# Performance work log

Hardware: AMD Instinct MI355X
Metric: run time of the kernel (lower is better)

## Reference

```python
import jax, jax.numpy as jnp
import numpy as np

NEG_SLOPE = 0.2
EPS = 1e-16


def _gat_layer(x, src, dst, W, a_src, a_dst, b, n_nodes):
    # x: [N, Fin], W: [Fout, Fin]; src/dst: [E'] (self-loops already appended)
    h = x @ W.T                              # [N, Fout]
    alpha_s = h @ a_src                      # [N] per-source score
    alpha_d = h @ a_dst                      # [N] per-dest score
    e = jax.nn.leaky_relu(alpha_s[src] + alpha_d[dst], NEG_SLOPE)  # [E']
    # segment softmax over destination nodes (PyG softmax semantics)
    m = jax.ops.segment_max(e, dst, num_segments=n_nodes)          # [N]
    ex = jnp.exp(e - m[dst])                                       # [E']
    s = jax.ops.segment_sum(ex, dst, num_segments=n_nodes)         # [N]
    alpha = ex / (s[dst] + EPS)                                    # [E']
    out = jax.ops.segment_sum(alpha[:, None] * h[src], dst, num_segments=n_nodes)
    return out + b, alpha


def setup_inputs() -> dict:
    key = jax.random.key(0)
    ks = jax.random.split(key, 14)
    N, E, F_IN, H1, H2, F_OUT = 50000, 800000, 128, 64, 64, 32
    sc = 0.1
    return {
        "x": jax.random.normal(ks[0], (N, F_IN), dtype=jnp.float32),
        "edge_index": jax.random.randint(ks[1], (2, E), 0, N, dtype=jnp.int64),
        "W1": jax.random.normal(ks[2], (H1, F_IN), dtype=jnp.float32) * sc,
        "a_src1": jax.random.normal(ks[3], (H1,), dtype=jnp.float32) * sc,
        "a_dst1": jax.random.normal(ks[4], (H1,), dtype=jnp.float32) * sc,
        "b1": jnp.zeros((H1,), dtype=jnp.float32),
        "W2": jax.random.normal(ks[5], (H2, H1), dtype=jnp.float32) * sc,
        "a_src2": jax.random.normal(ks[6], (H2,), dtype=jnp.float32) * sc,
        "a_dst2": jax.random.normal(ks[7], (H2,), dtype=jnp.float32) * sc,
        "b2": jnp.zeros((H2,), dtype=jnp.float32),
        "W3": jax.random.normal(ks[8], (F_OUT, H2), dtype=jnp.float32) * sc,
        "a_src3": jax.random.normal(ks[9], (F_OUT,), dtype=jnp.float32) * sc,
        "a_dst3": jax.random.normal(ks[10], (F_OUT,), dtype=jnp.float32) * sc,
        "b3": jnp.zeros((F_OUT,), dtype=jnp.float32),
    }


def reference(x, edge_index, W1, a_src1, a_dst1, b1, W2, a_src2, a_dst2, b2, W3, a_src3, a_dst3, b3):
    N = x.shape[0]
    loops = jnp.arange(N, dtype=edge_index.dtype)
    src = jnp.concatenate([edge_index[0], loops])  # add_self_loops=True
    dst = jnp.concatenate([edge_index[1], loops])

    h, alpha1 = _gat_layer(x, src, dst, W1, a_src1, a_dst1, b1, N)
    h = jax.nn.relu(h)
    h, _ = _gat_layer(h, src, dst, W2, a_src2, a_dst2, b2, N)
    h = jax.nn.relu(h)
    out, _ = _gat_layer(h, src, dst, W3, a_src3, a_dst3, b3, N)
    # att_tuple = (edge_index with self loops, attention coefficients of layer 1)
    return (jnp.stack([src, dst]), alpha1, out)
```

## Files before the change

kernel.cpp:

```cpp
#include <hip/hip_runtime.h>
#include <hip/hip_bf16.h>
#include <math.h>

#define NEG_SLOPE 0.2f
#define GAT_EPS 1e-16f

constexpr int NN = 50000;
constexpr int NE = 800000;
constexpr int EP = NE + NN;
constexpr int NB = (NN + 255) / 256;

__device__ inline void edge_sd(const int* __restrict__ ei, int i, int& s, int& d) {
    if (i < NE) { s = ei[i]; d = ei[NE + i]; }
    else        { s = d = i - NE; }
}

__device__ inline float bflo(unsigned int h) { return __uint_as_float(h << 16); }
__device__ inline float bfhi(unsigned int h) { return __uint_as_float(h & 0xffff0000u); }

__global__ void k_edges_hist(const int* __restrict__ ei, float* __restrict__ out0,
                             int* __restrict__ cnt, int* __restrict__ rank) {
    int i = blockIdx.x * blockDim.x + threadIdx.x;
    if (i >= EP) return;
    int s, d; edge_sd(ei, i, s, d);
    __builtin_nontemporal_store((float)s, &out0[i]);
    __builtin_nontemporal_store((float)d, &out0[EP + i]);
    int r = atomicAdd(&cnt[d], 1);
    __builtin_nontemporal_store(r, &rank[i]);
}

__global__ void k_scan1(const int* __restrict__ cnt, int* __restrict__ rowptr,
                        int* __restrict__ bsum) {
    __shared__ int sh[256];
    int t = threadIdx.x, i = blockIdx.x * 256 + t;
    int v = (i < NN) ? cnt[i] : 0;
    sh[t] = v; __syncthreads();
    for (int off = 1; off < 256; off <<= 1) {
        int x = (t >= off) ? sh[t - off] : 0;
        __syncthreads();
        sh[t] += x;
        __syncthreads();
    }
    if (i < NN) rowptr[i] = sh[t] - v;
    if (t == 255) bsum[blockIdx.x] = sh[255];
}

__global__ void k_scan2(int* __restrict__ bsum, int* __restrict__ boff) {
    __shared__ int sh[256];
    int t = threadIdx.x;
    int v = (t < NB) ? bsum[t] : 0;
    sh[t] = v; __syncthreads();
    for (int off = 1; off < 256; off <<= 1) {
        int x = (t >= off) ? sh[t - off] : 0;
        __syncthreads();
        sh[t] += x;
        __syncthreads();
    }
    if (t < NB) boff[t] = sh[t] - v;
}

__global__ void k_scan3(int* __restrict__ rowptr, const int* __restrict__ boff) {
    int i = blockIdx.x * blockDim.x + threadIdx.x;
    if (i < NN) rowptr[i] += boff[i >> 8];
    if (i == 0) rowptr[NN] = EP;
}

__global__ void k_fill(const int* __restrict__ ei, const int* __restrict__ rank,
                       const int* __restrict__ rowptr, int* __restrict__ col) {
    int i = blockIdx.x * blockDim.x + threadIdx.x;
    if (i >= EP) return;
    int s, d; edge_sd(ei, i, s, d);
    int pos = rowptr[d] + rank[i];
    __builtin_nontemporal_store(s, &col[pos]);
}

__global__ void k_alpha_out(const int* __restrict__ ei, const float* __restrict__ as_,
                            const float* __restrict__ ad_, const float* __restrict__ inv,
                            float* __restrict__ out_alpha) {
    int i = blockIdx.x * blockDim.x + threadIdx.x;
    if (i >= EP) return;
    int s, d; edge_sd(ei, i, s, d);
    float v = as_[s] + ad_[d];
    v = v > 0.f ? v : NEG_SLOPE * v;
    __builtin_nontemporal_store(__expf(v) * inv[d], &out_alpha[i]);
}

struct alignas(8) bh4 { __hip_bfloat16 a, b, c, d; };

__device__ inline void fma4(float4& acc, float x, const float4& w) {
    acc.x = fmaf(x, w.x, acc.x);
    acc.y = fmaf(x, w.y, acc.y);
    acc.z = fmaf(x, w.z, acc.z);
    acc.w = fmaf(x, w.w, acc.w);
}

template <int FIN, int FOUT, int NPB>
__global__ __launch_bounds__(256) void k_gemm_t(const float* __restrict__ in,
                                                const float* __restrict__ W,
                                                const float* __restrict__ avs,
                                                const float* __restrict__ avd,
                                                __hip_bfloat16* __restrict__ H,
                                                float* __restrict__ as_,
                                                float* __restrict__ ad_, int n) {
    constexpr int TF = FOUT / 4;
    constexpr int XS = FIN + 4;
    constexpr int WS = FOUT + 4;
    __shared__ float sX[NPB * XS];
    __shared__ float sWt[FIN * WS];
    int tid = threadIdx.x;
    for (int idx = tid; idx < FIN * FOUT; idx += 256) {
        int f = idx % FOUT, k = idx / FOUT;
        sWt[k * WS + f] = W[f * FIN + k];
    }
    int nb = blockIdx.x * NPB;
    for (int idx = tid; idx < NPB * (FIN / 4); idx += 256) {
        int node = idx / (FIN / 4), kq = idx % (FIN / 4);
        int g = nb + node;
        float4 v = make_float4(0.f, 0.f, 0.f, 0.f);
        if (g < n) v = *(const float4*)&in[(size_t)g * FIN + kq * 4];
        *(float4*)&sX[node * XS + kq * 4] = v;
    }
    __syncthreads();

    int fq = tid % TF, ng = tid / TF;
    int n0 = ng * 4;
    float4 acc0 = make_float4(0.f, 0.f, 0.f, 0.f);
    float4 acc1 = acc0, acc2 = acc0, acc3 = acc0;
    for (int k = 0; k < FIN; k += 4) {
        float4 w0 = *(const float4*)&sWt[(k + 0) * WS + fq * 4];
        float4 w1 = *(const float4*)&sWt[(k + 1) * WS + fq * 4];
        float4 w2 = *(const float4*)&sWt[(k + 2) * WS + fq * 4];
        float4 w3 = *(const float4*)&sWt[(k + 3) * WS + fq * 4];
        float4 x0 = *(const float4*)&sX[(n0 + 0) * XS + k];
        float4 x1 = *(const float4*)&sX[(n0 + 1) * XS + k];
        float4 x2 = *(const float4*)&sX[(n0 + 2) * XS + k];
        float4 x3 = *(const float4*)&sX[(n0 + 3) * XS + k];
        fma4(acc0, x0.x, w0); fma4(acc0, x0.y, w1); fma4(acc0, x0.z, w2); fma4(acc0, x0.w, w3);
        fma4(acc1, x1.x, w0); fma4(acc1, x1.y, w1); fma4(acc1, x1.z, w2); fma4(acc1, x1.w, w3);
        fma4(acc2, x2.x, w0); fma4(acc2, x2.y, w1); fma4(acc2, x2.z, w2); fma4(acc2, x2.w, w3);
        fma4(acc3, x3.x, w0); fma4(acc3, x3.y, w1); fma4(acc3, x3.z, w2); fma4(acc3, x3.w, w3);
    }
    float4 accs[4] = {acc0, acc1, acc2, acc3};
    float4 vs4 = *(const float4*)&avs[fq * 4];
    float4 vd4 = *(const float4*)&avd[fq * 4];
#pragma unroll
    for (int j = 0; j < 4; ++j) {
        int g = nb + n0 + j;
        float ps = accs[j].x * vs4.x + accs[j].y * vs4.y + accs[j].z * vs4.z + accs[j].w * vs4.w;
        float pd = accs[j].x * vd4.x + accs[j].y * vd4.y + accs[j].z * vd4.z + accs[j].w * vd4.w;
#pragma unroll
        for (int off = TF / 2; off; off >>= 1) {
            ps += __shfl_down(ps, off, TF);
            pd += __shfl_down(pd, off, TF);
        }
        if (g < n) {
            if (fq == 0) { as_[g] = ps; ad_[g] = pd; }
            bh4 o;
            o.a = __float2bfloat16(accs[j].x);
            o.b = __float2bfloat16(accs[j].y);
            o.c = __float2bfloat16(accs[j].z);
            o.d = __float2bfloat16(accs[j].w);
            *(bh4*)&H[(size_t)g * FOUT + fq * 4] = o;
        }
    }
}

template <int FOUT, bool RELU, bool WRITE_INV>
__global__ __launch_bounds__(256) void k_node_attn(
    const int* __restrict__ rowptr, const int* __restrict__ col,
    const float* __restrict__ as_, const float* __restrict__ ad_,
    const __hip_bfloat16* __restrict__ H, const float* __restrict__ bias,
    float* __restrict__ outp, float* __restrict__ inv_out) {
    int wid = (blockIdx.x * blockDim.x + threadIdx.x) >> 6;
    int lane = threadIdx.x & 63;
    if (wid >= NN) return;
    int start = rowptr[wid], end = rowptr[wid + 1];
    float adv = ad_[wid];
    const unsigned int* __restrict__ H2 = (const unsigned int*)H;

    float sloc = 0.f;
    float ax = 0.f, ay = 0.f;
    for (int c = start; c < end; c += 64) {
        int e = c + lane;
        float p = 0.f;
        int sc = 0;
        if (e < end) {
            sc = col[e];
            float v = as_[sc] + adv;
            v = v > 0.f ? v : NEG_SLOPE * v;
            p = __expf(v);
        }
        sloc += p;
        int cnt = end - c; if (cnt > 64) cnt = 64;
        if (FOUT == 64) {
            int half = lane >> 5, fl = lane & 31;
            int j = 0;
            for (; j + 8 <= cnt; j += 8) {
                int e0 = j + half, e1 = j + 2 + half, e2 = j + 4 + half, e3 = j + 6 + half;
                float p0 = __shfl(p, e0), p1 = __shfl(p, e1);
                float p2 = __shfl(p, e2), p3 = __shfl(p, e3);
                int s0 = __shfl(sc, e0), s1 = __shfl(sc, e1);
                int s2 = __shfl(sc, e2), s3 = __shfl(sc, e3);
                unsigned int h0 = H2[((size_t)s0 << 5) + fl];
                unsigned int h1 = H2[((size_t)s1 << 5) + fl];
                unsigned int h2 = H2[((size_t)s2 << 5) + fl];
                unsigned int h3 = H2[((size_t)s3 << 5) + fl];
                ax = fmaf(p0, bflo(h0), ax); ay = fmaf(p0, bfhi(h0), ay);
                ax = fmaf(p1, bflo(h1), ax); ay = fmaf(p1, bfhi(h1), ay);
                ax = fmaf(p2, bflo(h2), ax); ay = fmaf(p2, bfhi(h2), ay);
                ax = fmaf(p3, bflo(h3), ax); ay = fmaf(p3, bfhi(h3), ay);
            }
            for (; j < cnt; j += 2) {
                int e0 = j + half;
                float p0 = __shfl(p, e0);
                int   s0 = __shfl(sc, e0);
                unsigned int h0 = H2[((size_t)s0 << 5) + fl];
                ax = fmaf(p0, bflo(h0), ax); ay = fmaf(p0, bfhi(h0), ay);
            }
        } else {
            int q = lane >> 4, fl = lane & 15;
            int j = 0;
            for (; j + 16 <= cnt; j += 16) {
                int e0 = j + q, e1 = j + 4 + q, e2 = j + 8 + q, e3 = j + 12 + q;
                float p0 = __shfl(p, e0), p1 = __shfl(p, e1);
                float p2 = __shfl(p, e2), p3 = __shfl(p, e3);
                int s0 = __shfl(sc, e0), s1 = __shfl(sc, e1);
                int s2 = __shfl(sc, e2), s3 = __shfl(sc, e3);
                unsigned int h0 = H2[((size_t)s0 << 4) + fl];
                unsigned int h1 = H2[((size_t)s1 << 4) + fl];
                unsigned int h2 = H2[((size_t)s2 << 4) + fl];
                unsigned int h3 = H2[((size_t)s3 << 4) + fl];
                ax = fmaf(p0, bflo(h0), ax); ay = fmaf(p0, bfhi(h0), ay);
                ax = fmaf(p1, bflo(h1), ax); ay = fmaf(p1, bfhi(h1), ay);
                ax = fmaf(p2, bflo(h2), ax); ay = fmaf(p2, bfhi(h2), ay);
                ax = fmaf(p3, bflo(h3), ax); ay = fmaf(p3, bfhi(h3), ay);
            }
            for (; j < cnt; j += 4) {
                int e0 = j + q;
                float p0 = __shfl(p, e0);
                int   s0 = __shfl(sc, e0);
                unsigned int h0 = H2[((size_t)s0 << 4) + fl];
                ax = fmaf(p0, bflo(h0), ax); ay = fmaf(p0, bfhi(h0), ay);
            }
        }
    }
    for (int off = 32; off; off >>= 1) sloc += __shfl_xor(sloc, off);
    float inv = 1.f / (sloc + GAT_EPS);
    if (WRITE_INV && lane == 0) inv_out[wid] = inv;

    if (FOUT == 64) {
        ax += __shfl_xor(ax, 32);
        ay += __shfl_xor(ay, 32);
        if (lane < 32) {
            float2 bb = *(const float2*)&bias[lane * 2];
            float o0 = bb.x + ax * inv;
            float o1 = bb.y + ay * inv;
            if (RELU) { o0 = fmaxf(o0, 0.f); o1 = fmaxf(o1, 0.f); }
            *(float2*)&outp[((size_t)wid << 6) + lane * 2] = make_float2(o0, o1);
        }
    } else {
        ax += __shfl_xor(ax, 32); ay += __shfl_xor(ay, 32);
        ax += __shfl_xor(ax, 16); ay += __shfl_xor(ay, 16);
        if (lane < 16) {
            float2 bb = *(const float2*)&bias[lane * 2];
            float o0 = bb.x + ax * inv;
            float o1 = bb.y + ay * inv;
            if (RELU) { o0 = fmaxf(o0, 0.f); o1 = fmaxf(o1, 0.f); }
            *(float2*)&outp[((size_t)wid << 5) + lane * 2] = make_float2(o0, o1);
        }
    }
}

extern "C" void kernel_launch(void* const* d_in, const int* in_sizes, int n_in,
                              void* d_out, int out_size, void* d_ws, size_t ws_size,
                              hipStream_t stream) {
    const float* x  = (const float*)d_in[0];
    const int*   ei = (const int*)d_in[1];
    const float* W1 = (const float*)d_in[2];
    const float* as1 = (const float*)d_in[3];
    const float* ad1 = (const float*)d_in[4];
    const float* b1 = (const float*)d_in[5];
    const float* W2 = (const float*)d_in[6];
    const float* as2 = (const float*)d_in[7];
    const float* ad2 = (const float*)d_in[8];
    const float* b2 = (const float*)d_in[9];
    const float* W3 = (const float*)d_in[10];
    const float* as3 = (const float*)d_in[11];
    const float* ad3 = (const float*)d_in[12];
    const float* b3 = (const float*)d_in[13];

    float* out = (float*)d_out;
    float* out_edges = out;
    float* out_alpha = out + 2 * EP;
    float* out_final = out + 3 * EP;

    char* w = (char*)d_ws;
    size_t o = 0;
    float* as_ = (float*)(w + o); o += (size_t)NN * 4;
    float* ad_ = (float*)(w + o); o += (size_t)NN * 4;
    float* inv = (float*)(w + o); o += (size_t)NN * 4;
    __hip_bfloat16* H = (__hip_bfloat16*)(w + o); o += (size_t)NN * 64 * 2;
    int* rowptr = (int*)(w + o); o += ((size_t)(NN + 1) * 4 + 15) & ~15ull;
    int* cnt    = (int*)(w + o); o += (size_t)NN * 4;
    int* rank   = (int*)(w + o); o += (size_t)EP * 4;
    int* col    = (int*)(w + o); o += (size_t)EP * 4;
    int* bsum   = (int*)(w + o); o += 1024;
    int* boff   = (int*)(w + o); o += 1024;
    const size_t aggBytes = (size_t)NN * 64 * 4;
    float* agg = (ws_size >= o + aggBytes)
        ? (float*)(w + o)
        : (float*)d_in[0];

    hipMemsetAsync(cnt, 0, (size_t)NN * 4, stream);
    k_edges_hist<<<(EP + 255) / 256, 256, 0, stream>>>(ei, out_edges, cnt, rank);
    k_scan1<<<NB, 256, 0, stream>>>(cnt, rowptr, bsum);
    k_scan2<<<1, 256, 0, stream>>>(bsum, boff);
    k_scan3<<<NB, 256, 0, stream>>>(rowptr, boff);
    k_fill<<<(EP + 255) / 256, 256, 0, stream>>>(ei, rank, rowptr, col);

    const int nblk = (NN * 64 + 255) / 256;

    k_gemm_t<128, 64, 64><<<(NN + 63) / 64, 256, 0, stream>>>(x, W1, as1, ad1, H, as_, ad_, NN);
    k_node_attn<64, true, true><<<nblk, 256, 0, stream>>>(rowptr, col, as_, ad_, H, b1,
                                                          agg, inv);
    k_alpha_out<<<(EP + 255) / 256, 256, 0, stream>>>(ei, as_, ad_, inv, out_alpha);

    k_gemm_t<64, 64, 64><<<(NN + 63) / 64, 256, 0, stream>>>(agg, W2, as2, ad2, H, as_, ad_, NN);
    k_node_attn<64, true, false><<<nblk, 256, 0, stream>>>(rowptr, col, as_, ad_, H, b2,
                                                           agg, nullptr);

    k_gemm_t<64, 32, 128><<<(NN + 127) / 128, 256, 0, stream>>>(agg, W3, as3, ad3, H, as_, ad_,
                                                                NN);
    k_node_attn<32, false, false><<<nblk, 256, 0, stream>>>(rowptr, col, as_, ad_, H, b3,
                                                            out_final, nullptr);
}
```

Baseline: 327.2 us.

## Partition CSR build by XCD-sliced destination ranges and batch gather loads

The histogram and fill kernels are restructured so that each of 8 block groups (selected by blockIdx & 7, likely mapping to XCDs) only performs atomics on destinations in its own slice of nodes. The per-edge rank array is dropped: the fill now uses atomic cursors initialized from rowptr. The aim is to keep atomics local to one L2 and to save the rank write and read traffic. Each edge index is read up to 8 times, and CSR order within a row becomes nondeterministic. The gather loops are also unrolled to issue 8 independent H loads before the FMAs, giving more memory-level parallelism.

```diff
diff --git a/kernel.cpp b/kernel.cpp
--- a/kernel.cpp
+++ b/kernel.cpp
@@ -9,6 +9,10 @@
 constexpr int NE = 800000;
 constexpr int EP = NE + NN;
 constexpr int NB = (NN + 255) / 256;
+constexpr int SLICE = 6250;
+constexpr int HG = 416;
+constexpr int HSTRIDE = HG * 256;
+constexpr int OCHUNK = (EP + 7) / 8;
 
 __device__ inline void edge_sd(const int* __restrict__ ei, int i, int& s, int& d) {
     if (i < NE) { s = ei[i]; d = ei[NE + i]; }
@@ -18,15 +22,18 @@
 __device__ inline float bflo(unsigned int h) { return __uint_as_float(h << 16); }
 __device__ inline float bfhi(unsigned int h) { return __uint_as_float(h & 0xffff0000u); }
 
-__global__ void k_edges_hist(const int* __restrict__ ei, float* __restrict__ out0,
-                             int* __restrict__ cnt, int* __restrict__ rank) {
-    int i = blockIdx.x * blockDim.x + threadIdx.x;
-    if (i >= EP) return;
-    int s, d; edge_sd(ei, i, s, d);
-    __builtin_nontemporal_store((float)s, &out0[i]);
-    __builtin_nontemporal_store((float)d, &out0[EP + i]);
-    int r = atomicAdd(&cnt[d], 1);
-    __builtin_nontemporal_store(r, &rank[i]);
+__global__ void k_hist_x(const int* __restrict__ ei, float* __restrict__ out0,
+                         int* __restrict__ cnt) {
+    int g = blockIdx.x & 7;
+    int bi = blockIdx.x >> 3;
+    for (int i = bi * 256 + threadIdx.x; i < EP; i += HSTRIDE) {
+        int s, d; edge_sd(ei, i, s, d);
+        if (i / OCHUNK == g) {
+            __builtin_nontemporal_store((float)s, &out0[i]);
+            __builtin_nontemporal_store((float)d, &out0[EP + i]);
+        }
+        if ((unsigned)d / (unsigned)SLICE == (unsigned)g) atomicAdd(&cnt[d], 1);
+    }
 }
 
 __global__ void k_scan1(const int* __restrict__ cnt, int* __restrict__ rowptr,
@@ -59,19 +66,29 @@
     if (t < NB) boff[t] = sh[t] - v;
 }
 
-__global__ void k_scan3(int* __restrict__ rowptr, const int* __restrict__ boff) {
+__global__ void k_scan3(int* __restrict__ rowptr, const int* __restrict__ boff,
+                        int* __restrict__ wrt) {
     int i = blockIdx.x * blockDim.x + threadIdx.x;
-    if (i < NN) rowptr[i] += boff[i >> 8];
+    if (i < NN) {
+        int r = rowptr[i] + boff[i >> 8];
+        rowptr[i] = r;
+        wrt[i] = r;
+    }
     if (i == 0) rowptr[NN] = EP;
 }
 
-__global__ void k_fill(const int* __restrict__ ei, const int* __restrict__ rank,
-                       const int* __restrict__ rowptr, int* __restrict__ col) {
-    int i = blockIdx.x * blockDim.x + threadIdx.x;
-    if (i >= EP) return;
-    int s, d; edge_sd(ei, i, s, d);
-    int pos = rowptr[d] + rank[i];
-    __builtin_nontemporal_store(s, &col[pos]);
+__global__ void k_fill_x(const int* __restrict__ ei, int* __restrict__ wrt,
+                         int* __restrict__ col) {
+    int g = blockIdx.x & 7;
+    int bi = blockIdx.x >> 3;
+    for (int i = bi * 256 + threadIdx.x; i < EP; i += HSTRIDE) {
+        int d = (i < NE) ? ei[NE + i] : i - NE;
+        if ((unsigned)d / (unsigned)SLICE == (unsigned)g) {
+            int s = (i < NE) ? ei[i] : i - NE;
+            int pos = atomicAdd(&wrt[d], 1);
+            __builtin_nontemporal_store(s, &col[pos]);
+        }
+    }
 }
 
 __global__ void k_alpha_out(const int* __restrict__ ei, const float* __restrict__ as_,
@@ -195,20 +212,37 @@
         if (FOUT == 64) {
             int half = lane >> 5, fl = lane & 31;
             int j = 0;
+            for (; j + 16 <= cnt; j += 16) {
+                float pp[8]; int ss[8]; unsigned int hh[8];
+#pragma unroll
+                for (int k = 0; k < 8; ++k) {
+                    int ek = j + 2 * k + half;
+                    pp[k] = __shfl(p, ek);
+                    ss[k] = __shfl(sc, ek);
+                }
+#pragma unroll
+                for (int k = 0; k < 8; ++k) hh[k] = H2[((size_t)ss[k] << 5) + fl];
+#pragma unroll
+                for (int k = 0; k < 8; ++k) {
+                    ax = fmaf(pp[k], bflo(hh[k]), ax);
+                    ay = fmaf(pp[k], bfhi(hh[k]), ay);
+                }
+            }
             for (; j + 8 <= cnt; j += 8) {
-                int e0 = j + half, e1 = j + 2 + half, e2 = j + 4 + half, e3 = j + 6 + half;
-                float p0 = __shfl(p, e0), p1 = __shfl(p, e1);
-                float p2 = __shfl(p, e2), p3 = __shfl(p, e3);
-                int s0 = __shfl(sc, e0), s1 = __shfl(sc, e1);
-                int s2 = __shfl(sc, e2), s3 = __shfl(sc, e3);
-                unsigned int h0 = H2[((size_t)s0 << 5) + fl];
-                unsigned int h1 = H2[((size_t)s1 << 5) + fl];
-                unsigned int h2 = H2[((size_t)s2 << 5) + fl];
-                unsigned int h3 = H2[((size_t)s3 << 5) + fl];
-                ax = fmaf(p0, bflo(h0), ax); ay = fmaf(p0, bfhi(h0), ay);
-                ax = fmaf(p1, bflo(h1), ax); ay = fmaf(p1, bfhi(h1), ay);
-                ax = fmaf(p2, bflo(h2), ax); ay = fmaf(p2, bfhi(h2), ay);
-                ax = fmaf(p3, bflo(h3), ax); ay = fmaf(p3, bfhi(h3), ay);
+                float pp[4]; int ss[4]; unsigned int hh[4];
+#pragma unroll
+                for (int k = 0; k < 4; ++k) {
+                    int ek = j + 2 * k + half;
+                    pp[k] = __shfl(p, ek);
+                    ss[k] = __shfl(sc, ek);
+                }
+#pragma unroll
+                for (int k = 0; k < 4; ++k) hh[k] = H2[((size_t)ss[k] << 5) + fl];
+#pragma unroll
+                for (int k = 0; k < 4; ++k) {
+                    ax = fmaf(pp[k], bflo(hh[k]), ax);
+                    ay = fmaf(pp[k], bfhi(hh[k]), ay);
+                }
             }
             for (; j < cnt; j += 2) {
                 int e0 = j + half;
@@ -221,19 +255,20 @@
             int q = lane >> 4, fl = lane & 15;
             int j = 0;
             for (; j + 16 <= cnt; j += 16) {
-                int e0 = j + q, e1 = j + 4 + q, e2 = j + 8 + q, e3 = j + 12 + q;
-                float p0 = __shfl(p, e0), p1 = __shfl(p, e1);
-                float p2 = __shfl(p, e2), p3 = __shfl(p, e3);
-                int s0 = __shfl(sc, e0), s1 = __shfl(sc, e1);
-                int s2 = __shfl(sc, e2), s3 = __shfl(sc, e3);
-                unsigned int h0 = H2[((size_t)s0 << 4) + fl];
-                unsigned int h1 = H2[((size_t)s1 << 4) + fl];
-                unsigned int h2 = H2[((size_t)s2 << 4) + fl];
-                unsigned int h3 = H2[((size_t)s3 << 4) + fl];
-                ax = fmaf(p0, bflo(h0), ax); ay = fmaf(p0, bfhi(h0), ay);
-                ax = fmaf(p1, bflo(h1), ax); ay = fmaf(p1, bfhi(h1), ay);
-                ax = fmaf(p2, bflo(h2), ax); ay = fmaf(p2, bfhi(h2), ay);
-                ax = fmaf(p3, bflo(h3), ax); ay = fmaf(p3, bfhi(h3), ay);
+                float pp[4]; int ss[4]; unsigned int hh[4];
+#pragma unroll
+                for (int k = 0; k < 4; ++k) {
+                    int ek = j + 4 * k + q;
+                    pp[k] = __shfl(p, ek);
+                    ss[k] = __shfl(sc, ek);
+                }
+#pragma unroll
+                for (int k = 0; k < 4; ++k) hh[k] = H2[((size_t)ss[k] << 4) + fl];
+#pragma unroll
+                for (int k = 0; k < 4; ++k) {
+                    ax = fmaf(pp[k], bflo(hh[k]), ax);
+                    ay = fmaf(pp[k], bfhi(hh[k]), ay);
+                }
             }
             for (; j < cnt; j += 4) {
                 int e0 = j + q;
@@ -302,7 +337,6 @@
     __hip_bfloat16* H = (__hip_bfloat16*)(w + o); o += (size_t)NN * 64 * 2;
     int* rowptr = (int*)(w + o); o += ((size_t)(NN + 1) * 4 + 15) & ~15ull;
     int* cnt    = (int*)(w + o); o += (size_t)NN * 4;
-    int* rank   = (int*)(w + o); o += (size_t)EP * 4;
     int* col    = (int*)(w + o); o += (size_t)EP * 4;
     int* bsum   = (int*)(w + o); o += 1024;
     int* boff   = (int*)(w + o); o += 1024;
@@ -312,11 +346,11 @@
         : (float*)d_in[0];
 
     hipMemsetAsync(cnt, 0, (size_t)NN * 4, stream);
-    k_edges_hist<<<(EP + 255) / 256, 256, 0, stream>>>(ei, out_edges, cnt, rank);
+    k_hist_x<<<8 * HG, 256, 0, stream>>>(ei, out_edges, cnt);
     k_scan1<<<NB, 256, 0, stream>>>(cnt, rowptr, bsum);
     k_scan2<<<1, 256, 0, stream>>>(bsum, boff);
-    k_scan3<<<NB, 256, 0, stream>>>(rowptr, boff);
-    k_fill<<<(EP + 255) / 256, 256, 0, stream>>>(ei, rank, rowptr, col);
+    k_scan3<<<NB, 256, 0, stream>>>(rowptr, boff, cnt);
+    k_fill_x<<<8 * HG, 256, 0, stream>>>(ei, cnt, col);
 
     const int nblk = (NN * 64 + 255) / 256;
 
```

Measured after the change: 339.5 us. 1.04x slower.
